# Kernel tuning notes

Hardware: AMD Instinct MI355X
Metric: run time of the kernel (lower is better)

Reference implementation:

```python
import jax, jax.numpy as jnp
import numpy as np

IN = (8, 8, 8, 8)
OUT = (8, 8, 8, 8)
RANK = (1, 16, 16, 16, 1)  # boundary ranks = 1
BATCH = 4096


def setup_inputs() -> dict:
    key = jax.random.key(0)
    ks = jax.random.split(key, 5)
    x = jax.random.normal(ks[0], (BATCH, int(np.prod(IN))), dtype=jnp.float32)
    scale = 0.7  # matches nn.init.uniform_(f, -0.7, 0.7)
    factors = {}
    for k in range(4):
        shp = (RANK[k], OUT[k], IN[k], RANK[k + 1])
        factors[f"f{k}"] = jax.random.uniform(ks[k + 1], shp, jnp.float32, -scale, scale)
    bias = jnp.zeros((int(np.prod(OUT)),), dtype=jnp.float32)  # init.constant_(bias, 0)
    return {"x": x, **factors, "bias": bias}


def reference(x, f0, f1, f2, f3, bias):
    """TT-matrix linear: y = TT(W) @ x_vec + bias, cores of shape (r1, o, i, r2)."""
    cores = [f0, f1, f2, f3]
    B = x.shape[0]
    i0 = cores[0].shape[2]
    # t: (B, A=accumulated out dims, r=current rank, i=current in dim, X=remaining in dims)
    t = x.reshape(B, 1, 1, i0, -1)
    n = len(cores)
    for k, c in enumerate(cores):
        r1, o, i, r2 = c.shape
        # contract current rank and current input mode
        t = jnp.einsum('barix,rois->baosx', t, c)
        A = t.shape[1] * t.shape[2]
        X = t.shape[4]
        if k + 1 < n:
            i_next = cores[k + 1].shape[2]
            t = t.reshape(B, A, r2, i_next, X // i_next)
        else:
            t = t.reshape(B, A)  # r2 == 1, X == 1
    return t + bias
```

## Files before the change

kernel.cpp:

```cpp
#include <hip/hip_runtime.h>

typedef unsigned short u16;
typedef unsigned int u32;
typedef __attribute__((ext_vector_type(8))) short bf16x8;
typedef __attribute__((ext_vector_type(4))) float f32x4;

__device__ __forceinline__ u16 f2bf(float f) {
  u32 u = __float_as_uint(f);
  u += 0x7fffu + ((u >> 16) & 1u);
  return (u16)(u >> 16);
}

__global__ void prep_small(const float* __restrict__ f0, const float* __restrict__ f1,
                           const float* __restrict__ f2, const float* __restrict__ f3,
                           float* __restrict__ W01, float* __restrict__ W23) {
  int b = blockIdx.x;
  if (b < 256) {
    int idx = b * 256 + threadIdx.x;
    int r2 = idx & 15; int t = idx >> 4;
    int i1 = t & 7; t >>= 3;
    int i0 = t & 7; t >>= 3;
    int o1 = t & 7; int o0 = t >> 3;
    const float* a = f0 + (o0 * 8 + i0) * 16;
    const float* c = f1 + (o1 * 8 + i1) * 16 + r2;
    float s = 0.f;
#pragma unroll
    for (int r1 = 0; r1 < 16; ++r1) s += a[r1] * c[r1 * 1024];
    W01[idx] = s;
  } else {
    int idx = (b - 256) * 256 + threadIdx.x;
    int i3 = idx & 7, o3 = (idx >> 3) & 7, i2 = (idx >> 6) & 7;
    int o2 = (idx >> 9) & 7, r2 = idx >> 12;
    const float* a = f2 + ((r2 * 8 + o2) * 8 + i2) * 16;
    const float* c = f3 + o3 * 8 + i3;
    float s = 0.f;
#pragma unroll
    for (int r3 = 0; r3 < 16; ++r3) s += a[r3] * c[r3 * 64];
    W23[idx] = s;
  }
}

__global__ void prep_big(const float* __restrict__ W01, const float* __restrict__ W23,
                         const float* __restrict__ x, u16* __restrict__ W,
                         uint4* __restrict__ xb) {
  int b = blockIdx.x;
  if (b < 8192) {
    int idx = b * 256 + threadIdx.x;
    float4 a = ((const float4*)x)[idx * 2], d = ((const float4*)x)[idx * 2 + 1];
    union { u16 h[8]; uint4 v; } r;
    r.h[0] = f2bf(a.x); r.h[1] = f2bf(a.y); r.h[2] = f2bf(a.z); r.h[3] = f2bf(a.w);
    r.h[4] = f2bf(d.x); r.h[5] = f2bf(d.y); r.h[6] = f2bf(d.z); r.h[7] = f2bf(d.w);
    xb[idx] = r.v;
    return;
  }
  const int o = b - 8192;
  const int o2 = (o >> 3) & 7, o3 = o & 7;
  const int tid = threadIdx.x;
  __shared__ float sW23[1024];
  {
    int e = tid * 4;
    const float* src = W23 + (e >> 6) * 4096 + o2 * 512 + ((e >> 3) & 7) * 64
                         + o3 * 8 + (e & 7);
    ((float4*)sW23)[tid] = *(const float4*)src;
  }
  float w01r[16];
  {
    const float* a = W01 + (((o >> 6) * 64 + (tid >> 2)) << 4);
#pragma unroll
    for (int q = 0; q < 4; ++q) {
      float4 v = *(const float4*)(a + q * 4);
      w01r[q * 4] = v.x; w01r[q * 4 + 1] = v.y; w01r[q * 4 + 2] = v.z; w01r[q * 4 + 3] = v.w;
    }
  }
  __syncthreads();

  const int i2a = 2 * (tid & 3), i2b = i2a + 1;
  float acc[16] = {};
#pragma unroll
  for (int r2 = 0; r2 < 16; ++r2) {
    const float w = w01r[r2];
    const float4 va0 = *(const float4*)(sW23 + r2 * 64 + i2a * 8);
    const float4 va1 = *(const float4*)(sW23 + r2 * 64 + i2a * 8 + 4);
    const float4 vb0 = *(const float4*)(sW23 + r2 * 64 + i2b * 8);
    const float4 vb1 = *(const float4*)(sW23 + r2 * 64 + i2b * 8 + 4);
    acc[0]  += w * va0.x; acc[1]  += w * va0.y; acc[2]  += w * va0.z; acc[3]  += w * va0.w;
    acc[4]  += w * va1.x; acc[5]  += w * va1.y; acc[6]  += w * va1.z; acc[7]  += w * va1.w;
    acc[8]  += w * vb0.x; acc[9]  += w * vb0.y; acc[10] += w * vb0.z; acc[11] += w * vb0.w;
    acc[12] += w * vb1.x; acc[13] += w * vb1.y; acc[14] += w * vb1.z; acc[15] += w * vb1.w;
  }
  union { u16 h[8]; uint4 v; } r0, r1;
#pragma unroll
  for (int j = 0; j < 8; ++j) { r0.h[j] = f2bf(acc[j]); r1.h[j] = f2bf(acc[8 + j]); }
  uint4* dst = (uint4*)(W + (size_t)o * 4096 + tid * 16);
  dst[0] = r0.v; dst[1] = r1.v;
}

__device__ __forceinline__ void gload_lds16(const void* g, void* l) {
  __builtin_amdgcn_global_load_lds((__attribute__((address_space(1))) void*)(g),
                                   (__attribute__((address_space(3))) void*)(l),
                                   16, 0, 0);
}

__global__ __launch_bounds__(256, 2) void gemm256(
    const u16* __restrict__ A, const u16* __restrict__ B,
    const float* __restrict__ bias, float* __restrict__ C) {
  constexpr int K = 4096, N = 4096, NT = 128;
  __shared__ u16 S[24576];
  const int tid  = threadIdx.x;
  const int wave = tid >> 6, lane = tid & 63;
  const int l15 = lane & 15, l4 = lane >> 4;
  const int wr = wave >> 1, wc = wave & 1;
  const int bm = (int)(blockIdx.x >> 5) * 256;
  const int bn = (int)(blockIdx.x & 31) * 128;

  const int ls = (tid & 3) ^ ((tid >> 3) & 3);
  const int rr = tid >> 2;
  const u16* srcA0 = A + (size_t)(bm +       rr) * K + ls * 8;
  const u16* srcA1 = A + (size_t)(bm +  64 + rr) * K + ls * 8;
  const u16* srcA2 = A + (size_t)(bm + 128 + rr) * K + ls * 8;
  const u16* srcA3 = A + (size_t)(bm + 192 + rr) * K + ls * 8;
  const u16* srcB0 = B + (size_t)(bn +       rr) * K + ls * 8;
  const u16* srcB1 = B + (size_t)(bn +  64 + rr) * K + ls * 8;
  const int d8 = tid * 8;

  int offA[8], offB[4];
#pragma unroll
  for (int mi = 0; mi < 8; ++mi) {
    int r = wr * 128 + mi * 16 + l15;
    offA[mi] = r * 32 + ((l4 ^ ((r >> 1) & 3)) * 8);
  }
#pragma unroll
  for (int ni = 0; ni < 4; ++ni) {
    int r = wc * 64 + ni * 16 + l15;
    offB[ni] = 8192 + r * 32 + ((l4 ^ ((r >> 1) & 3)) * 8);
  }

#define STAGE(kts, slot) do { u16* _b = S + (slot) * 12288;                      \
    gload_lds16(srcA0 + (size_t)(kts) * 32, _b + d8);                            \
    gload_lds16(srcA1 + (size_t)(kts) * 32, _b + 2048 + d8);                     \
    gload_lds16(srcA2 + (size_t)(kts) * 32, _b + 4096 + d8);                     \
    gload_lds16(srcA3 + (size_t)(kts) * 32, _b + 6144 + d8);                     \
    gload_lds16(srcB0 + (size_t)(kts) * 32, _b + 8192 + d8);                     \
    gload_lds16(srcB1 + (size_t)(kts) * 32, _b + 10240 + d8); } while (0)

  STAGE(0, 0);
  asm volatile("s_waitcnt vmcnt(0)");
  __builtin_amdgcn_s_barrier();

  f32x4 acc[8][4] = {};

  for (int kt = 0; kt < NT; ++kt) {
    const u16* base = S + (kt & 1) * 12288;

    bf16x8 av[4], avN[4], bv[4];
#pragma unroll
    for (int i = 0; i < 4; ++i) av[i]  = *(const bf16x8*)(base + offA[i]);
#pragma unroll
    for (int i = 0; i < 4; ++i) bv[i]  = *(const bf16x8*)(base + offB[i]);
#pragma unroll
    for (int i = 0; i < 4; ++i) avN[i] = *(const bf16x8*)(base + offA[4 + i]);
    STAGE((kt + 1) & (NT - 1), (kt & 1) ^ 1);

#pragma unroll
    for (int mi = 0; mi < 4; ++mi)
#pragma unroll
      for (int ni = 0; ni < 4; ++ni)
        acc[mi][ni] = __builtin_amdgcn_mfma_f32_16x16x32_bf16(
            av[mi], bv[ni], acc[mi][ni], 0, 0, 0);
#pragma unroll
    for (int mi = 0; mi < 4; ++mi)
#pragma unroll
      for (int ni = 0; ni < 4; ++ni)
        acc[4 + mi][ni] = __builtin_amdgcn_mfma_f32_16x16x32_bf16(
            avN[mi], bv[ni], acc[4 + mi][ni], 0, 0, 0);

    __builtin_amdgcn_sched_group_barrier(0x100, 8, 0);
    __builtin_amdgcn_sched_group_barrier(0x008, 4, 0);
    __builtin_amdgcn_sched_group_barrier(0x100, 4, 0);
    __builtin_amdgcn_sched_group_barrier(0x008, 4, 0);
    __builtin_amdgcn_sched_group_barrier(0x070, 6, 0);
    __builtin_amdgcn_sched_group_barrier(0x008, 24, 0);

    asm volatile("s_waitcnt vmcnt(0)");
    __builtin_amdgcn_s_barrier();
  }

#pragma unroll
  for (int ni = 0; ni < 4; ++ni) {
    const int col = bn + wc * 64 + ni * 16 + l15;
    const float bvs = bias[col];
#pragma unroll
    for (int mi = 0; mi < 8; ++mi) {
      const int row0 = bm + wr * 128 + mi * 16 + l4 * 4;
#pragma unroll
      for (int j = 0; j < 4; ++j)
        C[(size_t)(row0 + j) * N + col] = acc[mi][ni][j] + bvs;
    }
  }
  asm volatile("s_waitcnt vmcnt(0)" ::: "memory");
#undef STAGE
}

extern "C" void kernel_launch(void* const* d_in, const int* in_sizes, int n_in,
                              void* d_out, int out_size, void* d_ws, size_t ws_size,
                              hipStream_t stream) {
  const float* x    = (const float*)d_in[0];
  const float* f0   = (const float*)d_in[1];
  const float* f1   = (const float*)d_in[2];
  const float* f2   = (const float*)d_in[3];
  const float* f3   = (const float*)d_in[4];
  const float* bias = (const float*)d_in[5];

  char* ws = (char*)d_ws;
  u16* Wb = (u16*)(ws);
  u16* xb = (u16*)(ws + 33554432);
  float* W01 = (float*)d_out;
  float* W23 = (float*)d_out + 65536;

  prep_small<<<512,   256, 0, stream>>>(f0, f1, f2, f3, W01, W23);
  prep_big  <<<12288, 256, 0, stream>>>(W01, W23, x, Wb, (uint4*)xb);
  gemm256   <<<512,   256, 0, stream>>>(xb, Wb, bias, (float*)d_out);
}
```

Measured before the change: 170.9 us.

## Triple-buffer LDS in GEMM with prefetch depth two and interleaved schedule

Moves the GEMM main loop from double to triple buffering in shared memory. Each iteration now prefetches tile kt+2 and waits only for the older batch of loads (vmcnt(6)), so global-to-LDS latency is spread over two iterations. The sched_group_barrier pattern is rewritten to interleave the MFMAs more finely with the LDS reads and global loads. LDS use per block rises from 48KB to 72KB, which may limit how many blocks fit per CU alongside launch_bounds(256,2).

```diff
diff --git a/kernel.cpp b/kernel.cpp
--- a/kernel.cpp
+++ b/kernel.cpp
@@ -105,7 +105,7 @@
     const u16* __restrict__ A, const u16* __restrict__ B,
     const float* __restrict__ bias, float* __restrict__ C) {
   constexpr int K = 4096, N = 4096, NT = 128;
-  __shared__ u16 S[24576];
+  __shared__ u16 S[36864];
   const int tid  = threadIdx.x;
   const int wave = tid >> 6, lane = tid & 63;
   const int l15 = lane & 15, l4 = lane >> 4;
@@ -135,7 +135,7 @@
     offB[ni] = 8192 + r * 32 + ((l4 ^ ((r >> 1) & 3)) * 8);
   }
 
-#define STAGE(kts, slot) do { u16* _b = S + (slot) * 12288;                      \
+#define STAGE(kts, sbase) do { u16* _b = (sbase);                                \
     gload_lds16(srcA0 + (size_t)(kts) * 32, _b + d8);                            \
     gload_lds16(srcA1 + (size_t)(kts) * 32, _b + 2048 + d8);                     \
     gload_lds16(srcA2 + (size_t)(kts) * 32, _b + 4096 + d8);                     \
@@ -143,23 +143,22 @@
     gload_lds16(srcB0 + (size_t)(kts) * 32, _b + 8192 + d8);                     \
     gload_lds16(srcB1 + (size_t)(kts) * 32, _b + 10240 + d8); } while (0)
 
-  STAGE(0, 0);
-  asm volatile("s_waitcnt vmcnt(0)");
+  STAGE(0, S); STAGE(1, S + 12288);
+  asm volatile("s_waitcnt vmcnt(6)");
   __builtin_amdgcn_s_barrier();
 
   f32x4 acc[8][4] = {};
+  u16 *cur = S, *nxt = S + 12288, *stg = S + 24576;
 
   for (int kt = 0; kt < NT; ++kt) {
-    const u16* base = S + (kt & 1) * 12288;
-
     bf16x8 av[4], avN[4], bv[4];
 #pragma unroll
-    for (int i = 0; i < 4; ++i) av[i]  = *(const bf16x8*)(base + offA[i]);
-#pragma unroll
-    for (int i = 0; i < 4; ++i) bv[i]  = *(const bf16x8*)(base + offB[i]);
-#pragma unroll
-    for (int i = 0; i < 4; ++i) avN[i] = *(const bf16x8*)(base + offA[4 + i]);
-    STAGE((kt + 1) & (NT - 1), (kt & 1) ^ 1);
+    for (int i = 0; i < 4; ++i) av[i]  = *(const bf16x8*)(cur + offA[i]);
+#pragma unroll
+    for (int i = 0; i < 4; ++i) bv[i]  = *(const bf16x8*)(cur + offB[i]);
+#pragma unroll
+    for (int i = 0; i < 4; ++i) avN[i] = *(const bf16x8*)(cur + offA[4 + i]);
+    STAGE((kt + 2) & (NT - 1), stg);
 
 #pragma unroll
     for (int mi = 0; mi < 4; ++mi)
@@ -174,15 +173,34 @@
         acc[4 + mi][ni] = __builtin_amdgcn_mfma_f32_16x16x32_bf16(
             avN[mi], bv[ni], acc[4 + mi][ni], 0, 0, 0);
 
-    __builtin_amdgcn_sched_group_barrier(0x100, 8, 0);
-    __builtin_amdgcn_sched_group_barrier(0x008, 4, 0);
-    __builtin_amdgcn_sched_group_barrier(0x100, 4, 0);
-    __builtin_amdgcn_sched_group_barrier(0x008, 4, 0);
-    __builtin_amdgcn_sched_group_barrier(0x070, 6, 0);
-    __builtin_amdgcn_sched_group_barrier(0x008, 24, 0);
-
-    asm volatile("s_waitcnt vmcnt(0)");
+    __builtin_amdgcn_sched_group_barrier(0x100, 1, 0);
+    __builtin_amdgcn_sched_group_barrier(0x008, 2, 0);
+    __builtin_amdgcn_sched_group_barrier(0x100, 2, 0);
+    __builtin_amdgcn_sched_group_barrier(0x008, 2, 0);
+    __builtin_amdgcn_sched_group_barrier(0x070, 2, 0);
+    __builtin_amdgcn_sched_group_barrier(0x008, 4, 0);
+    __builtin_amdgcn_sched_group_barrier(0x100, 1, 0);
+    __builtin_amdgcn_sched_group_barrier(0x008, 2, 0);
+    __builtin_amdgcn_sched_group_barrier(0x100, 2, 0);
+    __builtin_amdgcn_sched_group_barrier(0x008, 2, 0);
+    __builtin_amdgcn_sched_group_barrier(0x070, 1, 0);
+    __builtin_amdgcn_sched_group_barrier(0x008, 4, 0);
+    __builtin_amdgcn_sched_group_barrier(0x100, 1, 0);
+    __builtin_amdgcn_sched_group_barrier(0x008, 2, 0);
+    __builtin_amdgcn_sched_group_barrier(0x100, 2, 0);
+    __builtin_amdgcn_sched_group_barrier(0x008, 2, 0);
+    __builtin_amdgcn_sched_group_barrier(0x070, 2, 0);
+    __builtin_amdgcn_sched_group_barrier(0x008, 4, 0);
+    __builtin_amdgcn_sched_group_barrier(0x100, 1, 0);
+    __builtin_amdgcn_sched_group_barrier(0x008, 2, 0);
+    __builtin_amdgcn_sched_group_barrier(0x100, 2, 0);
+    __builtin_amdgcn_sched_group_barrier(0x008, 2, 0);
+    __builtin_amdgcn_sched_group_barrier(0x070, 1, 0);
+    __builtin_amdgcn_sched_group_barrier(0x008, 4, 0);
+
+    asm volatile("s_waitcnt vmcnt(6)");
     __builtin_amdgcn_s_barrier();
+    u16* t = cur; cur = nxt; nxt = stg; stg = t;
   }
 
 #pragma unroll
```

After: 166.3 us. 2.7% less time.
